# Optimization experiments

Hardware: AMD Instinct MI355X
Metric: run time of the kernel (lower is better)

The kernel has to match this reference:

```python
import jax, jax.numpy as jnp
import numpy as np

B = 512          # graphs
NODES = 90       # nodes per graph (fixed by lin1 = Linear(90*L*H, ...))
N = B * NODES    # total nodes
F_IN = 90        # dataset.num_features
H = 128          # hidden
L = 3            # num_layers
HL = 64          # hidden_linear
C = 2            # dataset.num_classes
DEG = 16         # avg degree
E = N * DEG      # total edges


def setup_inputs() -> dict:
    key = jax.random.key(0)
    ks = jax.random.split(key, 14)
    x = jax.random.normal(ks[0], (N, F_IN), jnp.float32)
    # intra-graph random edges: graph g owns nodes [g*90, (g+1)*90)
    g = jnp.repeat(jnp.arange(B), NODES * DEG)
    src = g * NODES + jax.random.randint(ks[1], (E,), 0, NODES)
    dst = g * NODES + jax.random.randint(ks[2], (E,), 0, NODES)
    edge_index = jnp.stack([src, dst]).astype(jnp.int64)
    edge_attr = jax.random.uniform(ks[3], (E,), jnp.float32, 0.1, 1.0)
    batch = jnp.repeat(jnp.arange(B), NODES).astype(jnp.int64)

    def lin(k, fi, fo):
        s = 1.0 / np.sqrt(fi)
        kw, kb = jax.random.split(k)
        return (jax.random.uniform(kw, (fi, fo), jnp.float32, -s, s),
                jax.random.uniform(kb, (fo,), jnp.float32, -s, s))

    W1, b1 = lin(ks[4], F_IN, H)
    W2, b2 = lin(ks[5], H, H)
    W3, b3 = lin(ks[6], H, H)
    lin1_W, lin1_b = lin(ks[7], NODES * L * H, HL)
    lin2_W, lin2_b = lin(ks[8], HL, C)
    return {"x": x, "edge_attr": edge_attr, "W1": W1, "b1": b1, "W2": W2,
            "b2": b2, "W3": W3, "b3": b3, "lin1_W": lin1_W, "lin1_b": lin1_b,
            "lin2_W": lin2_W, "lin2_b": lin2_b, "edge_index": edge_index,
            "batch": batch}


def reference(x, edge_attr, W1, b1, W2, b2, W3, b3, lin1_W, lin1_b,
              lin2_W, lin2_b, edge_index, batch):
    src, dst = edge_index[0], edge_index[1]
    # GCN normalization with added self-loops (weight 1), as in PyG GCNConv
    loop = jnp.arange(N)
    s = jnp.concatenate([src, loop])
    d = jnp.concatenate([dst, loop])
    w = jnp.concatenate([edge_attr, jnp.ones((N,), x.dtype)])
    deg = jax.ops.segment_sum(w, d, num_segments=N)
    dis = jnp.where(deg > 0, jax.lax.rsqrt(jnp.maximum(deg, 1e-30)), 0.0)
    norm = dis[s] * w * dis[d]  # [E+N]

    def conv(h, W, b):
        h = h @ W                                  # [N, H]
        msg = norm[:, None] * h[s]                 # gather+scale [E+N, H]
        return jax.ops.segment_sum(msg, d, num_segments=N) + b

    h1 = jax.nn.relu(conv(x, W1, b1))
    h2 = jax.nn.relu(conv(h1, W2, b2))
    h3 = jax.nn.relu(conv(h2, W3, b3))
    xc = jnp.concatenate([h1, h2, h3], axis=1)     # [N, L*H]
    # to_dense_batch: every graph has exactly 90 nodes in order, so no padding
    # (fill_value never appears) and dense batching is a pure reshape.
    z = xc.reshape(B, NODES * L * H)
    h = jax.nn.relu(z @ lin1_W + lin1_b)
    logits = h @ lin2_W + lin2_b                   # dropout is identity in eval
    return jax.nn.log_softmax(logits, axis=-1)
```

## Files before the change

kernel.cpp:

```cpp
#include <hip/hip_runtime.h>

typedef __bf16 bfx8 __attribute__((ext_vector_type(8)));
typedef float fx4 __attribute__((ext_vector_type(4)));
typedef unsigned short us4 __attribute__((ext_vector_type(4)));
typedef unsigned short us8 __attribute__((ext_vector_type(8)));

#define NNODES 90
#define NPAD   96
#define HF     128
#define NGRAPH 512
#define EPG    1440
#define ETOT   (NGRAPH*EPG)
#define KTOT   34560
#define NKTOT  1080
#define KSPLIT 45
#define KSTEPS (NKTOT/KSPLIT)

__device__ __forceinline__ float bf2f(unsigned short s){
  union { unsigned u; float f; } v; v.u = ((unsigned)s)<<16; return v.f;
}
__device__ __forceinline__ unsigned short f2bf(float f){
  union { float f; unsigned u; } v; v.f = f;
  return (unsigned short)((v.u + 0x7FFFu + ((v.u>>16)&1u)) >> 16);
}

__global__ void probe_kern(const unsigned short* __restrict__ x,
                           const int* __restrict__ ei,
                           int* __restrict__ flags){
  int t = threadIdx.x;
  __shared__ int sw[4];
  __shared__ long long se;
  int weird = 0;
  for (int i = t; i < 1024; i += 256) {
    unsigned u = x[i];
    int ex = (u >> 7) & 0xFF;
    if (ex > 157 || (ex < 97 && u != 0)) weird++;
  }
  for (int off = 32; off; off >>= 1) weird += __shfl_down(weird, off);
  if ((t & 63) == 0) sw[t >> 6] = weird;
  long long ss = 0;
  if (t < 64) { int v = ei[2*t + 1]; ss = (v < 0) ? -(long long)v : (long long)v; }
  for (int off = 32; off; off >>= 1) ss += __shfl_down(ss, off);
  if (t == 0) se = ss;
  __syncthreads();
  if (t == 0) {
    flags[0] = ((sw[0]+sw[1]+sw[2]+sw[3]) > 100) ? 1 : 0;
    flags[1] = (se == 0) ? 1 : 0;
  }
}

__global__ void pack_w3_kern(const unsigned short* __restrict__ W1,
                             const unsigned short* __restrict__ W2,
                             const unsigned short* __restrict__ W3,
                             unsigned short* __restrict__ o1,
                             unsigned short* __restrict__ o2,
                             unsigned short* __restrict__ o3,
                             const int* __restrict__ flags){
  int b = blockIdx.x;
  const unsigned short* W; unsigned short* out; int K, nK, t;
  if (b < 6)       { W = W1; out = o1; K = 90;  nK = 3; t = b*256 + threadIdx.x; }
  else if (b < 14) { W = W2; out = o2; K = 128; nK = 4; t = (b-6)*256 + threadIdx.x; }
  else             { W = W3; out = o3; K = 128; nK = 4; t = (b-14)*256 + threadIdx.x; }
  const int f32f = flags[0];
  const float* Wf = (const float*)W;
  int lane = t & 63;
  int ks = (t>>6) % nK;
  int nt = (t>>6) / nK;
  int n  = nt*16 + (lane&15);
  int k0 = ks*32 + (lane>>4)*8;
  unsigned short v[8];
#pragma unroll
  for (int j=0;j<8;j++){
    int k=k0+j;
    unsigned short val = 0;
    if (k < K) val = f32f ? f2bf(Wf[k*128+n]) : W[k*128+n];
    v[j] = val;
  }
  unsigned short* o = out + ((nt*nK+ks)*64 + lane)*8;
#pragma unroll
  for (int j=0;j<8;j++) o[j]=v[j];
}

__global__ void pack_lin1_kern(const unsigned short* __restrict__ W,
                               unsigned short* __restrict__ out,
                               const int* __restrict__ flags){
  __shared__ __align__(16) unsigned short tile[32*64];
  int ks = blockIdx.x;
  int t  = threadIdx.x;
  const int f32f = flags[0];
  if (f32f) {
    const float* Wf = (const float*)W;
#pragma unroll
    for (int j=0;j<8;j++) tile[t*8+j] = f2bf(Wf[ks*32*64 + t*8 + j]);
  } else {
    us8 v = *(const us8*)&W[ks*32*64 + t*8];
    *(us8*)&tile[t*8] = v;
  }
  __syncthreads();
  int lane = t & 63;
  int nt = t >> 6;
  int n  = nt*16 + (lane&15);
  int kq = (lane>>4)*8;
  us8 v;
#pragma unroll
  for (int j=0;j<8;j++) v[j] = tile[(kq+j)*64 + n];
  *(us8*)&out[((nt*NKTOT + ks)*64 + lane)*8] = v;
}

__global__ __launch_bounds__(512) void gcn_layers_kern(
    const unsigned short* __restrict__ x,
    const unsigned short* __restrict__ eattr,
    const int* __restrict__ ei,
    const unsigned short* __restrict__ w1p,
    const unsigned short* __restrict__ w2p,
    const unsigned short* __restrict__ w3p,
    const unsigned short* __restrict__ b1,
    const unsigned short* __restrict__ b2,
    const unsigned short* __restrict__ b3,
    unsigned short* __restrict__ xc,
    const int* __restrict__ flags)
{
  __shared__ __align__(16) char smem[65280];
  unsigned short* Abf = (unsigned short*)smem;
  unsigned short* H   = (unsigned short*)(smem + 17280);
  unsigned short* Tt  = (unsigned short*)(smem + 40320);
  float* Af  = (float*)(smem + 17280);
  float* deg = (float*)(smem + 64896);

  const int g = blockIdx.x;
  const int tid = threadIdx.x;
  const int lane = tid & 63, wave = tid >> 6;
  const int q = lane >> 4, r = lane & 15;
  const int eb = g*EPG;
  const int nb = g*NNODES;
  const int f32f = flags[0];
  const int i64f = flags[1];
  const float* xf = (const float*)x;
  const float* eaf = (const float*)eattr;
  const long long* e64 = (const long long*)ei;

  for (int i = tid; i < NNODES; i += 512) deg[i] = 1.0f;
  for (int i = tid; i < NNODES*NPAD; i += 512) Af[i] = 0.0f;
  __syncthreads();
  for (int e = tid; e < EPG; e += 512) {
    int d = (i64f ? (int)e64[ETOT + eb + e] : ei[ETOT + eb + e]) - nb;
    float w = f32f ? eaf[eb + e] : bf2f(eattr[eb + e]);
    atomicAdd(&deg[d], w);
  }
  __syncthreads();
  for (int i = tid; i < NNODES; i += 512) deg[i] = rsqrtf(deg[i]);
  __syncthreads();
  for (int e = tid; e < EPG; e += 512) {
    int s = (i64f ? (int)e64[eb + e] : ei[eb + e]) - nb;
    int d = (i64f ? (int)e64[ETOT + eb + e] : ei[ETOT + eb + e]) - nb;
    float w = f32f ? eaf[eb + e] : bf2f(eattr[eb + e]);
    atomicAdd(&Af[d*NPAD + s], deg[d]*w*deg[s]);
  }
  for (int i = tid; i < NNODES; i += 512) atomicAdd(&Af[i*NPAD + i], deg[i]*deg[i]);
  __syncthreads();
  for (int i = tid; i < NNODES*NPAD; i += 512) Abf[i] = f2bf(Af[i]);
  __syncthreads();
  for (int i = tid; i < NNODES*90; i += 512) {
    int node = i/90, f = i - node*90;
    H[node*HF + f] = f32f ? f2bf(xf[(nb + node)*90 + f]) : x[(nb + node)*90 + f];
  }
  for (int i = tid; i < NNODES*6; i += 512) {
    int node = i/6, c = i - node*6;
    H[node*HF + 90 + c] = 0;
  }
  __syncthreads();

#pragma unroll
  for (int l = 0; l < 3; ++l) {
    const unsigned short* wpk  = (l==0)? w1p : (l==1)? w2p : w3p;
    const unsigned short* bias = (l==0)? b1 : (l==1)? b2 : b3;
    const int nK = (l==0)? 3 : 4;

    {
      const int nt = wave;
      for (int mt = 0; mt < 6; ++mt) {
        int row = mt*16 + r; if (row > 89) row = 89;
        fx4 acc = {0.f,0.f,0.f,0.f};
#pragma unroll
        for (int ks = 0; ks < 4; ++ks)
          if (ks < nK) {
            bfx8 af = *(const bfx8*)(const void*)&H[row*HF + ks*32 + q*8];
            bfx8 bf = *(const bfx8*)(const void*)&wpk[((nt*nK + ks)*64 + lane)*8];
            acc = __builtin_amdgcn_mfma_f32_16x16x32_bf16(af, bf, acc, 0,0,0);
          }
        us4 o;
#pragma unroll
        for (int i2=0;i2<4;i2++) o[i2] = f2bf(acc[i2]);
        *(us4*)&Tt[(nt*16 + r)*NPAD + mt*16 + q*4] = o;
      }
    }
    __syncthreads();

    {
      const int ft = wave;
      bfx8 af[3];
#pragma unroll
      for (int ks = 0; ks < 3; ++ks)
        af[ks] = *(const bfx8*)(const void*)&Tt[(ft*16 + r)*NPAD + ks*32 + q*8];
      float bv[4];
#pragma unroll
      for (int i2=0;i2<4;i2++){
        int bidx = ft*16 + q*4 + i2;
        bv[i2] = f32f ? ((const float*)bias)[bidx] : bf2f(bias[bidx]);
      }
      for (int nt = 0; nt < 6; ++nt) {
        int arow = nt*16 + r; if (arow > 89) arow = 89;
        fx4 acc = {0.f,0.f,0.f,0.f};
#pragma unroll
        for (int ks = 0; ks < 3; ++ks) {
          bfx8 bfr = *(const bfx8*)(const void*)&Abf[arow*NPAD + ks*32 + q*8];
          acc = __builtin_amdgcn_mfma_f32_16x16x32_bf16(af[ks], bfr, acc, 0,0,0);
        }
        int m = nt*16 + r;
        if (m < NNODES) {
          us4 o;
#pragma unroll
          for (int i2=0;i2<4;i2++){
            float v = acc[i2] + bv[i2];
            o[i2] = f2bf(v > 0.f ? v : 0.f);
          }
          *(us4*)&H[m*HF + ft*16 + q*4] = o;
        }
      }
    }
    __syncthreads();

    for (int i = tid*4; i < NNODES*HF; i += 512*4) {
      us4 v = *(const us4*)&H[i];
      int node = i >> 7, f = i & 127;
      *(us4*)&xc[(nb + node)*384 + l*128 + f] = v;
    }
    __syncthreads();
  }
}

__global__ __launch_bounds__(256) void gemm2_kern(
    const unsigned short* __restrict__ z,
    const unsigned short* __restrict__ wp,
    float* __restrict__ accf)
{
  __shared__ __align__(16) unsigned short zt[32*128];
  int mb = blockIdx.x % 16;
  int kb = blockIdx.x / 16;
  int tid = threadIdx.x;
  int lane = tid & 63, wave = tid >> 6;
  int q = lane >> 4, r = lane & 15;
  int mt = wave >> 1;
  int nt0 = (wave & 1)*2;
  int m0 = mb*32;

  fx4 acc0 = {0,0,0,0}, acc1 = {0,0,0,0};
  int Lm = tid >> 3, Lc = tid & 7;
  int cA = Lc ^ (Lm & 7);
  int arow = mt*16 + r;

  for (int it = 0; it < KSTEPS/4; ++it) {
    int ks0 = kb*KSTEPS + it*4;
    int kbase = ks0*32;
    {
      us8 vA = *(const us8*)&z[(m0+Lm)*KTOT + kbase + cA*8];
      us8 vB = *(const us8*)&z[(m0+Lm)*KTOT + kbase + (cA+8)*8];
      *(us8*)&zt[Lm*128 + Lc*8] = vA;
      *(us8*)&zt[Lm*128 + (Lc+8)*8] = vB;
    }
    __syncthreads();
#pragma unroll
    for (int ks2 = 0; ks2 < 4; ++ks2) {
      int c = ks2*4 + q;
      int pos = (c & 8) | ((c & 7) ^ (arow & 7));
      bfx8 af = *(const bfx8*)(const void*)&zt[arow*128 + pos*8];
      int ksg = ks0 + ks2;
      bfx8 bA = *(const bfx8*)(const void*)&wp[(((nt0+0)*NKTOT + ksg)*64 + lane)*8];
      bfx8 bB = *(const bfx8*)(const void*)&wp[(((nt0+1)*NKTOT + ksg)*64 + lane)*8];
      acc0 = __builtin_amdgcn_mfma_f32_16x16x32_bf16(af, bA, acc0, 0,0,0);
      acc1 = __builtin_amdgcn_mfma_f32_16x16x32_bf16(af, bB, acc1, 0,0,0);
    }
    __syncthreads();
  }
#pragma unroll
  for (int i2 = 0; i2 < 4; ++i2) {
    int row = m0 + mt*16 + q*4 + i2;
    atomicAdd(&accf[row*64 + (nt0+0)*16 + r], acc0[i2]);
    atomicAdd(&accf[row*64 + (nt0+1)*16 + r], acc1[i2]);
  }
}

__global__ void head_kern(const float* __restrict__ accf,
                          const unsigned short* __restrict__ l1b,
                          const unsigned short* __restrict__ l2w,
                          const unsigned short* __restrict__ l2b,
                          unsigned short* __restrict__ out,
                          const int* __restrict__ flags)
{
  int gph = blockIdx.x;
  int j = threadIdx.x;
  const int f32f = flags[0];
  const float* l1bf = (const float*)l1b;
  const float* l2wf = (const float*)l2w;
  const float* l2bf = (const float*)l2b;
  float h = accf[gph*64 + j] + (f32f ? l1bf[j] : bf2f(l1b[j]));
  h = h > 0.f ? h : 0.f;
  float p0 = h * (f32f ? l2wf[2*j]   : bf2f(l2w[2*j]));
  float p1 = h * (f32f ? l2wf[2*j+1] : bf2f(l2w[2*j+1]));
  for (int off = 32; off; off >>= 1) {
    p0 += __shfl_down(p0, off);
    p1 += __shfl_down(p1, off);
  }
  if (j == 0) {
    float l0 = p0 + (f32f ? l2bf[0] : bf2f(l2b[0]));
    float l1 = p1 + (f32f ? l2bf[1] : bf2f(l2b[1]));
    float mx = fmaxf(l0, l1);
    float lse = mx + logf(expf(l0-mx) + expf(l1-mx));
    if (f32f) {
      ((float*)out)[gph*2]   = l0 - lse;
      ((float*)out)[gph*2+1] = l1 - lse;
    } else {
      out[gph*2]   = f2bf(l0 - lse);
      out[gph*2+1] = f2bf(l1 - lse);
    }
  }
}

extern "C" void kernel_launch(void* const* d_in, const int* in_sizes, int n_in,
                              void* d_out, int out_size, void* d_ws, size_t ws_size,
                              hipStream_t stream)
{
  const unsigned short* x   = (const unsigned short*)d_in[0];
  const unsigned short* ea  = (const unsigned short*)d_in[1];
  const unsigned short* W1  = (const unsigned short*)d_in[2];
  const unsigned short* b1  = (const unsigned short*)d_in[3];
  const unsigned short* W2  = (const unsigned short*)d_in[4];
  const unsigned short* b2  = (const unsigned short*)d_in[5];
  const unsigned short* W3  = (const unsigned short*)d_in[6];
  const unsigned short* b3  = (const unsigned short*)d_in[7];
  const unsigned short* L1W = (const unsigned short*)d_in[8];
  const unsigned short* L1b = (const unsigned short*)d_in[9];
  const unsigned short* L2W = (const unsigned short*)d_in[10];
  const unsigned short* L2b = (const unsigned short*)d_in[11];
  const int* ei             = (const int*)d_in[12];
  unsigned short* out       = (unsigned short*)d_out;

  char* ws = (char*)d_ws;
  unsigned short* xc  = (unsigned short*)(ws);
  unsigned short* l1p = (unsigned short*)(ws + 35389440);
  unsigned short* w1p = (unsigned short*)(ws + 39813120);
  unsigned short* w2p = (unsigned short*)(ws + 39837696);
  unsigned short* w3p = (unsigned short*)(ws + 39870464);
  float* accf         = (float*)(ws + 39903232);
  int* flags          = (int*)(ws + 40034304);

  probe_kern<<<1, 256, 0, stream>>>(x, ei, flags);
  pack_w3_kern<<<22, 256, 0, stream>>>(W1, W2, W3, w1p, w2p, w3p, flags);
  pack_lin1_kern<<<NKTOT, 256, 0, stream>>>(L1W, l1p, flags);
  gcn_layers_kern<<<NGRAPH, 512, 0, stream>>>(x, ea, ei, w1p, w2p, w3p,
                                              b1, b2, b3, xc, flags);
  hipMemsetAsync(accf, 0, NGRAPH*64*sizeof(float), stream);
  gemm2_kern<<<16*KSPLIT, 256, 0, stream>>>(xc, l1p, accf);
  head_kern<<<NGRAPH, 64, 0, stream>>>(accf, L1b, L2W, L2b, out, flags);
}
```

Measured before the change: 171.5 us.

## Merge pack kernels, drop dtype probe, swizzle H, prefetch gemm2 tiles

Removes the runtime dtype probe kernel and fixes inputs as fp32. The weight-pack kernels and the accumulator memset are merged into one launch. In the GCN kernel, the edge lists are loaded once into registers and the degree and adjacency atomics are fused, with normalization applied when converting to bf16. H uses an XOR-swizzled LDS layout to avoid bank conflicts, and per-layer weights are hoisted into registers. The lin1 GEMM register-prefetches the next z tile, and the head kernel packs 4 graphs per block. Fewer launches and less LDS contention are the aim. The cost is dropping the bf16 input path.

```diff
diff --git a/kernel.cpp b/kernel.cpp
--- a/kernel.cpp
+++ b/kernel.cpp
@@ -16,109 +16,79 @@
 #define KSPLIT 45
 #define KSTEPS (NKTOT/KSPLIT)
 
-__device__ __forceinline__ float bf2f(unsigned short s){
-  union { unsigned u; float f; } v; v.u = ((unsigned)s)<<16; return v.f;
-}
 __device__ __forceinline__ unsigned short f2bf(float f){
   union { float f; unsigned u; } v; v.f = f;
   return (unsigned short)((v.u + 0x7FFFu + ((v.u>>16)&1u)) >> 16);
 }
-
-__global__ void probe_kern(const unsigned short* __restrict__ x,
-                           const int* __restrict__ ei,
-                           int* __restrict__ flags){
+__device__ __forceinline__ int hsw(int node, int f){
+  return node*HF + ((((f>>3) ^ (node&15)))<<3) + (f&7);
+}
+
+__global__ __launch_bounds__(256) void pack_all_kern(
+    const float* __restrict__ W1,
+    const float* __restrict__ W2,
+    const float* __restrict__ W3,
+    const float* __restrict__ L1W,
+    unsigned short* __restrict__ o1,
+    unsigned short* __restrict__ o2,
+    unsigned short* __restrict__ o3,
+    unsigned short* __restrict__ l1p,
+    float* __restrict__ accf)
+{
+  __shared__ __align__(16) unsigned short tile[32*64];
+  int b = blockIdx.x;
   int t = threadIdx.x;
-  __shared__ int sw[4];
-  __shared__ long long se;
-  int weird = 0;
-  for (int i = t; i < 1024; i += 256) {
-    unsigned u = x[i];
-    int ex = (u >> 7) & 0xFF;
-    if (ex > 157 || (ex < 97 && u != 0)) weird++;
-  }
-  for (int off = 32; off; off >>= 1) weird += __shfl_down(weird, off);
-  if ((t & 63) == 0) sw[t >> 6] = weird;
-  long long ss = 0;
-  if (t < 64) { int v = ei[2*t + 1]; ss = (v < 0) ? -(long long)v : (long long)v; }
-  for (int off = 32; off; off >>= 1) ss += __shfl_down(ss, off);
-  if (t == 0) se = ss;
-  __syncthreads();
-  if (t == 0) {
-    flags[0] = ((sw[0]+sw[1]+sw[2]+sw[3]) > 100) ? 1 : 0;
-    flags[1] = (se == 0) ? 1 : 0;
-  }
-}
-
-__global__ void pack_w3_kern(const unsigned short* __restrict__ W1,
-                             const unsigned short* __restrict__ W2,
-                             const unsigned short* __restrict__ W3,
-                             unsigned short* __restrict__ o1,
-                             unsigned short* __restrict__ o2,
-                             unsigned short* __restrict__ o3,
-                             const int* __restrict__ flags){
-  int b = blockIdx.x;
-  const unsigned short* W; unsigned short* out; int K, nK, t;
-  if (b < 6)       { W = W1; out = o1; K = 90;  nK = 3; t = b*256 + threadIdx.x; }
-  else if (b < 14) { W = W2; out = o2; K = 128; nK = 4; t = (b-6)*256 + threadIdx.x; }
-  else             { W = W3; out = o3; K = 128; nK = 4; t = (b-14)*256 + threadIdx.x; }
-  const int f32f = flags[0];
-  const float* Wf = (const float*)W;
-  int lane = t & 63;
-  int ks = (t>>6) % nK;
-  int nt = (t>>6) / nK;
-  int n  = nt*16 + (lane&15);
-  int k0 = ks*32 + (lane>>4)*8;
-  unsigned short v[8];
-#pragma unroll
-  for (int j=0;j<8;j++){
-    int k=k0+j;
-    unsigned short val = 0;
-    if (k < K) val = f32f ? f2bf(Wf[k*128+n]) : W[k*128+n];
-    v[j] = val;
-  }
-  unsigned short* o = out + ((nt*nK+ks)*64 + lane)*8;
-#pragma unroll
-  for (int j=0;j<8;j++) o[j]=v[j];
-}
-
-__global__ void pack_lin1_kern(const unsigned short* __restrict__ W,
-                               unsigned short* __restrict__ out,
-                               const int* __restrict__ flags){
-  __shared__ __align__(16) unsigned short tile[32*64];
-  int ks = blockIdx.x;
-  int t  = threadIdx.x;
-  const int f32f = flags[0];
-  if (f32f) {
-    const float* Wf = (const float*)W;
-#pragma unroll
-    for (int j=0;j<8;j++) tile[t*8+j] = f2bf(Wf[ks*32*64 + t*8 + j]);
+  if (b < NKTOT) {
+    int ks = b;
+#pragma unroll
+    for (int j=0;j<8;j++) tile[t*8+j] = f2bf(L1W[ks*32*64 + t*8 + j]);
+    __syncthreads();
+    int lane = t & 63;
+    int nt = t >> 6;
+    int n  = nt*16 + (lane&15);
+    int kq = (lane>>4)*8;
+    us8 v;
+#pragma unroll
+    for (int j=0;j<8;j++) v[j] = tile[(kq+j)*64 + n];
+    *(us8*)&l1p[((nt*NKTOT + ks)*64 + lane)*8] = v;
+  } else if (b < NKTOT + 22) {
+    int bb = b - NKTOT;
+    const float* W; unsigned short* out; int K, nK, tt;
+    if (bb < 6)       { W = W1; out = o1; K = 90;  nK = 3; tt = bb*256 + t; }
+    else if (bb < 14) { W = W2; out = o2; K = 128; nK = 4; tt = (bb-6)*256 + t; }
+    else              { W = W3; out = o3; K = 128; nK = 4; tt = (bb-14)*256 + t; }
+    int lane = tt & 63;
+    int ks = (tt>>6) % nK;
+    int nt = (tt>>6) / nK;
+    int n  = nt*16 + (lane&15);
+    int k0 = ks*32 + (lane>>4)*8;
+    unsigned short v[8];
+#pragma unroll
+    for (int j=0;j<8;j++){ int k=k0+j; v[j] = (k<K)? f2bf(W[k*128+n]) : (unsigned short)0; }
+    unsigned short* o = out + ((nt*nK+ks)*64 + lane)*8;
+#pragma unroll
+    for (int j=0;j<8;j++) o[j]=v[j];
   } else {
-    us8 v = *(const us8*)&W[ks*32*64 + t*8];
-    *(us8*)&tile[t*8] = v;
-  }
-  __syncthreads();
-  int lane = t & 63;
-  int nt = t >> 6;
-  int n  = nt*16 + (lane&15);
-  int kq = (lane>>4)*8;
-  us8 v;
-#pragma unroll
-  for (int j=0;j<8;j++) v[j] = tile[(kq+j)*64 + n];
-  *(us8*)&out[((nt*NKTOT + ks)*64 + lane)*8] = v;
+    int base = (b - (NKTOT+22))*16384 + t*4;
+#pragma unroll
+    for (int i = 0; i < 16; ++i) {
+      fx4 z = {0.f,0.f,0.f,0.f};
+      *(fx4*)&accf[base + i*1024] = z;
+    }
+  }
 }
 
 __global__ __launch_bounds__(512) void gcn_layers_kern(
-    const unsigned short* __restrict__ x,
-    const unsigned short* __restrict__ eattr,
+    const float* __restrict__ x,
+    const float* __restrict__ eattr,
     const int* __restrict__ ei,
     const unsigned short* __restrict__ w1p,
     const unsigned short* __restrict__ w2p,
     const unsigned short* __restrict__ w3p,
-    const unsigned short* __restrict__ b1,
-    const unsigned short* __restrict__ b2,
-    const unsigned short* __restrict__ b3,
-    unsigned short* __restrict__ xc,
-    const int* __restrict__ flags)
+    const float* __restrict__ b1,
+    const float* __restrict__ b2,
+    const float* __restrict__ b3,
+    unsigned short* __restrict__ xc)
 {
   __shared__ __align__(16) char smem[65280];
   unsigned short* Abf = (unsigned short*)smem;
@@ -133,88 +103,98 @@
   const int q = lane >> 4, r = lane & 15;
   const int eb = g*EPG;
   const int nb = g*NNODES;
-  const int f32f = flags[0];
-  const int i64f = flags[1];
-  const float* xf = (const float*)x;
-  const float* eaf = (const float*)eattr;
   const long long* e64 = (const long long*)ei;
 
-  for (int i = tid; i < NNODES; i += 512) deg[i] = 1.0f;
+  bool i64f;
+  {
+    int v = ei[2*lane + 1];
+    i64f = (__ballot(v != 0) == 0ull);
+  }
+
+  const int e0 = tid, e1 = tid + 512, e2 = tid + 1024;
+  const bool h2 = (e2 < EPG);
+  int s0, d0, s1, d1, s2 = nb, d2 = nb;
+  if (i64f) {
+    s0 = (int)e64[eb+e0]; d0 = (int)e64[ETOT+eb+e0];
+    s1 = (int)e64[eb+e1]; d1 = (int)e64[ETOT+eb+e1];
+    if (h2) { s2 = (int)e64[eb+e2]; d2 = (int)e64[ETOT+eb+e2]; }
+  } else {
+    s0 = ei[eb+e0]; d0 = ei[ETOT+eb+e0];
+    s1 = ei[eb+e1]; d1 = ei[ETOT+eb+e1];
+    if (h2) { s2 = ei[eb+e2]; d2 = ei[ETOT+eb+e2]; }
+  }
+  float w0 = eattr[eb+e0];
+  float w1 = eattr[eb+e1];
+  float w2 = h2 ? eattr[eb+e2] : 0.f;
+
+  for (int i = tid; i < NPAD; i += 512) deg[i] = 1.0f;
   for (int i = tid; i < NNODES*NPAD; i += 512) Af[i] = 0.0f;
   __syncthreads();
-  for (int e = tid; e < EPG; e += 512) {
-    int d = (i64f ? (int)e64[ETOT + eb + e] : ei[ETOT + eb + e]) - nb;
-    float w = f32f ? eaf[eb + e] : bf2f(eattr[eb + e]);
-    atomicAdd(&deg[d], w);
-  }
-  __syncthreads();
-  for (int i = tid; i < NNODES; i += 512) deg[i] = rsqrtf(deg[i]);
-  __syncthreads();
-  for (int e = tid; e < EPG; e += 512) {
-    int s = (i64f ? (int)e64[eb + e] : ei[eb + e]) - nb;
-    int d = (i64f ? (int)e64[ETOT + eb + e] : ei[ETOT + eb + e]) - nb;
-    float w = f32f ? eaf[eb + e] : bf2f(eattr[eb + e]);
-    atomicAdd(&Af[d*NPAD + s], deg[d]*w*deg[s]);
-  }
-  for (int i = tid; i < NNODES; i += 512) atomicAdd(&Af[i*NPAD + i], deg[i]*deg[i]);
-  __syncthreads();
-  for (int i = tid; i < NNODES*NPAD; i += 512) Abf[i] = f2bf(Af[i]);
+  atomicAdd(&Af[(d0-nb)*NPAD + (s0-nb)], w0); atomicAdd(&deg[d0-nb], w0);
+  atomicAdd(&Af[(d1-nb)*NPAD + (s1-nb)], w1); atomicAdd(&deg[d1-nb], w1);
+  if (h2) { atomicAdd(&Af[(d2-nb)*NPAD + (s2-nb)], w2); atomicAdd(&deg[d2-nb], w2); }
+  __syncthreads();
+  for (int i = tid; i < NPAD; i += 512) deg[i] = rsqrtf(deg[i]);
+  __syncthreads();
+  for (int i = tid; i < NNODES*NPAD; i += 512) {
+    int row = i / NPAD, col = i - row*NPAD;
+    float a = Af[i];
+    if (col == row) a += 1.0f;
+    Abf[i] = f2bf(a * deg[row] * deg[col]);
+  }
   __syncthreads();
   for (int i = tid; i < NNODES*90; i += 512) {
     int node = i/90, f = i - node*90;
-    H[node*HF + f] = f32f ? f2bf(xf[(nb + node)*90 + f]) : x[(nb + node)*90 + f];
+    H[hsw(node, f)] = f2bf(x[(nb + node)*90 + f]);
   }
   for (int i = tid; i < NNODES*6; i += 512) {
-    int node = i/6, c = i - node*6;
-    H[node*HF + 90 + c] = 0;
+    int node = i/6, f = 90 + (i - node*6);
+    H[hsw(node, f)] = 0;
   }
   __syncthreads();
 
 #pragma unroll
   for (int l = 0; l < 3; ++l) {
-    const unsigned short* wpk  = (l==0)? w1p : (l==1)? w2p : w3p;
-    const unsigned short* bias = (l==0)? b1 : (l==1)? b2 : b3;
+    const unsigned short* wpk = (l==0)? w1p : (l==1)? w2p : w3p;
+    const float* bias         = (l==0)? b1 : (l==1)? b2 : b3;
     const int nK = (l==0)? 3 : 4;
 
+    bfx8 wf[4];
+#pragma unroll
+    for (int ks = 0; ks < 4; ++ks)
+      if (ks < nK) wf[ks] = *(const bfx8*)(const void*)&wpk[((wave*nK + ks)*64 + lane)*8];
+
+    for (int mt = 0; mt < 6; ++mt) {
+      int row = mt*16 + r; if (row > 89) row = 89;
+      fx4 acc = {0.f,0.f,0.f,0.f};
+#pragma unroll
+      for (int ks = 0; ks < 4; ++ks)
+        if (ks < nK) {
+          bfx8 af = *(const bfx8*)(const void*)&H[row*HF + (((4*ks + q) ^ (row&15))<<3)];
+          acc = __builtin_amdgcn_mfma_f32_16x16x32_bf16(af, wf[ks], acc, 0,0,0);
+        }
+      us4 o;
+#pragma unroll
+      for (int i2=0;i2<4;i2++) o[i2] = f2bf(acc[i2]);
+      *(us4*)&Tt[(wave*16 + r)*NPAD + mt*16 + q*4] = o;
+    }
+    __syncthreads();
+
     {
-      const int nt = wave;
-      for (int mt = 0; mt < 6; ++mt) {
-        int row = mt*16 + r; if (row > 89) row = 89;
-        fx4 acc = {0.f,0.f,0.f,0.f};
-#pragma unroll
-        for (int ks = 0; ks < 4; ++ks)
-          if (ks < nK) {
-            bfx8 af = *(const bfx8*)(const void*)&H[row*HF + ks*32 + q*8];
-            bfx8 bf = *(const bfx8*)(const void*)&wpk[((nt*nK + ks)*64 + lane)*8];
-            acc = __builtin_amdgcn_mfma_f32_16x16x32_bf16(af, bf, acc, 0,0,0);
-          }
-        us4 o;
-#pragma unroll
-        for (int i2=0;i2<4;i2++) o[i2] = f2bf(acc[i2]);
-        *(us4*)&Tt[(nt*16 + r)*NPAD + mt*16 + q*4] = o;
-      }
-    }
-    __syncthreads();
-
-    {
-      const int ft = wave;
-      bfx8 af[3];
+      bfx8 tf[3];
 #pragma unroll
       for (int ks = 0; ks < 3; ++ks)
-        af[ks] = *(const bfx8*)(const void*)&Tt[(ft*16 + r)*NPAD + ks*32 + q*8];
+        tf[ks] = *(const bfx8*)(const void*)&Tt[(wave*16 + r)*NPAD + ks*32 + q*8];
       float bv[4];
 #pragma unroll
-      for (int i2=0;i2<4;i2++){
-        int bidx = ft*16 + q*4 + i2;
-        bv[i2] = f32f ? ((const float*)bias)[bidx] : bf2f(bias[bidx]);
-      }
+      for (int i2=0;i2<4;i2++) bv[i2] = bias[wave*16 + q*4 + i2];
       for (int nt = 0; nt < 6; ++nt) {
         int arow = nt*16 + r; if (arow > 89) arow = 89;
         fx4 acc = {0.f,0.f,0.f,0.f};
 #pragma unroll
         for (int ks = 0; ks < 3; ++ks) {
           bfx8 bfr = *(const bfx8*)(const void*)&Abf[arow*NPAD + ks*32 + q*8];
-          acc = __builtin_amdgcn_mfma_f32_16x16x32_bf16(af[ks], bfr, acc, 0,0,0);
+          acc = __builtin_amdgcn_mfma_f32_16x16x32_bf16(tf[ks], bfr, acc, 0,0,0);
         }
         int m = nt*16 + r;
         if (m < NNODES) {
@@ -224,18 +204,17 @@
             float v = acc[i2] + bv[i2];
             o[i2] = f2bf(v > 0.f ? v : 0.f);
           }
-          *(us4*)&H[m*HF + ft*16 + q*4] = o;
+          *(us4*)&H[m*HF + (((2*wave + (q>>1)) ^ (m&15))<<3) + (q&1)*4] = o;
         }
       }
     }
     __syncthreads();
 
     for (int i = tid*4; i < NNODES*HF; i += 512*4) {
-      us4 v = *(const us4*)&H[i];
       int node = i >> 7, f = i & 127;
+      us4 v = *(const us4*)&H[node*HF + (((f>>3) ^ (node&15))<<3) + (f&7)];
       *(us4*)&xc[(nb + node)*384 + l*128 + f] = v;
     }
-    __syncthreads();
   }
 }
 
@@ -258,17 +237,21 @@
   int Lm = tid >> 3, Lc = tid & 7;
   int cA = Lc ^ (Lm & 7);
   int arow = mt*16 + r;
+  const unsigned short* zrow = &z[(m0+Lm)*KTOT];
+
+  us8 pvA = *(const us8*)&zrow[kb*KSTEPS*32 + cA*8];
+  us8 pvB = *(const us8*)&zrow[kb*KSTEPS*32 + (cA+8)*8];
 
   for (int it = 0; it < KSTEPS/4; ++it) {
+    *(us8*)&zt[Lm*128 + Lc*8] = pvA;
+    *(us8*)&zt[Lm*128 + (Lc+8)*8] = pvB;
+    __syncthreads();
+    if (it < KSTEPS/4 - 1) {
+      int kn = (kb*KSTEPS + (it+1)*4)*32;
+      pvA = *(const us8*)&zrow[kn + cA*8];
+      pvB = *(const us8*)&zrow[kn + (cA+8)*8];
+    }
     int ks0 = kb*KSTEPS + it*4;
-    int kbase = ks0*32;
-    {
-      us8 vA = *(const us8*)&z[(m0+Lm)*KTOT + kbase + cA*8];
-      us8 vB = *(const us8*)&z[(m0+Lm)*KTOT + kbase + (cA+8)*8];
-      *(us8*)&zt[Lm*128 + Lc*8] = vA;
-      *(us8*)&zt[Lm*128 + (Lc+8)*8] = vB;
-    }
-    __syncthreads();
 #pragma unroll
     for (int ks2 = 0; ks2 < 4; ++ks2) {
       int c = ks2*4 + q;
@@ -290,39 +273,30 @@
   }
 }
 
-__global__ void head_kern(const float* __restrict__ accf,
-                          const unsigned short* __restrict__ l1b,
-                          const unsigned short* __restrict__ l2w,
-                          const unsigned short* __restrict__ l2b,
-                          unsigned short* __restrict__ out,
-                          const int* __restrict__ flags)
-{
-  int gph = blockIdx.x;
-  int j = threadIdx.x;
-  const int f32f = flags[0];
-  const float* l1bf = (const float*)l1b;
-  const float* l2wf = (const float*)l2w;
-  const float* l2bf = (const float*)l2b;
-  float h = accf[gph*64 + j] + (f32f ? l1bf[j] : bf2f(l1b[j]));
+__global__ __launch_bounds__(256) void head_kern(
+    const float* __restrict__ accf,
+    const float* __restrict__ l1b,
+    const float* __restrict__ l2w,
+    const float* __restrict__ l2b,
+    float* __restrict__ out)
+{
+  int gph = blockIdx.x*4 + (threadIdx.x >> 6);
+  int j = threadIdx.x & 63;
+  float h = accf[gph*64 + j] + l1b[j];
   h = h > 0.f ? h : 0.f;
-  float p0 = h * (f32f ? l2wf[2*j]   : bf2f(l2w[2*j]));
-  float p1 = h * (f32f ? l2wf[2*j+1] : bf2f(l2w[2*j+1]));
+  float p0 = h * l2w[2*j];
+  float p1 = h * l2w[2*j+1];
   for (int off = 32; off; off >>= 1) {
     p0 += __shfl_down(p0, off);
     p1 += __shfl_down(p1, off);
   }
   if (j == 0) {
-    float l0 = p0 + (f32f ? l2bf[0] : bf2f(l2b[0]));
-    float l1 = p1 + (f32f ? l2bf[1] : bf2f(l2b[1]));
+    float l0 = p0 + l2b[0];
+    float l1 = p1 + l2b[1];
     float mx = fmaxf(l0, l1);
     float lse = mx + logf(expf(l0-mx) + expf(l1-mx));
-    if (f32f) {
-      ((float*)out)[gph*2]   = l0 - lse;
-      ((float*)out)[gph*2+1] = l1 - lse;
-    } else {
-      out[gph*2]   = f2bf(l0 - lse);
-      out[gph*2+1] = f2bf(l1 - lse);
-    }
+    out[gph*2]   = l0 - lse;
+    out[gph*2+1] = l1 - lse;
   }
 }
 
@@ -330,20 +304,20 @@
                               void* d_out, int out_size, void* d_ws, size_t ws_size,
                               hipStream_t stream)
 {
-  const unsigned short* x   = (const unsigned short*)d_in[0];
-  const unsigned short* ea  = (const unsigned short*)d_in[1];
-  const unsigned short* W1  = (const unsigned short*)d_in[2];
-  const unsigned short* b1  = (const unsigned short*)d_in[3];
-  const unsigned short* W2  = (const unsigned short*)d_in[4];
-  const unsigned short* b2  = (const unsigned short*)d_in[5];
-  const unsigned short* W3  = (const unsigned short*)d_in[6];
-  const unsigned short* b3  = (const unsigned short*)d_in[7];
-  const unsigned short* L1W = (const unsigned short*)d_in[8];
-  const unsigned short* L1b = (const unsigned short*)d_in[9];
-  const unsigned short* L2W = (const unsigned short*)d_in[10];
-  const unsigned short* L2b = (const unsigned short*)d_in[11];
-  const int* ei             = (const int*)d_in[12];
-  unsigned short* out       = (unsigned short*)d_out;
+  const float* x   = (const float*)d_in[0];
+  const float* ea  = (const float*)d_in[1];
+  const float* W1  = (const float*)d_in[2];
+  const float* b1  = (const float*)d_in[3];
+  const float* W2  = (const float*)d_in[4];
+  const float* b2  = (const float*)d_in[5];
+  const float* W3  = (const float*)d_in[6];
+  const float* b3  = (const float*)d_in[7];
+  const float* L1W = (const float*)d_in[8];
+  const float* L1b = (const float*)d_in[9];
+  const float* L2W = (const float*)d_in[10];
+  const float* L2b = (const float*)d_in[11];
+  const int* ei    = (const int*)d_in[12];
+  float* out       = (float*)d_out;
 
   char* ws = (char*)d_ws;
   unsigned short* xc  = (unsigned short*)(ws);
@@ -352,14 +326,11 @@
   unsigned short* w2p = (unsigned short*)(ws + 39837696);
   unsigned short* w3p = (unsigned short*)(ws + 39870464);
   float* accf         = (float*)(ws + 39903232);
-  int* flags          = (int*)(ws + 40034304);
-
-  probe_kern<<<1, 256, 0, stream>>>(x, ei, flags);
-  pack_w3_kern<<<22, 256, 0, stream>>>(W1, W2, W3, w1p, w2p, w3p, flags);
-  pack_lin1_kern<<<NKTOT, 256, 0, stream>>>(L1W, l1p, flags);
+
+  pack_all_kern<<<NKTOT + 22 + 2, 256, 0, stream>>>(W1, W2, W3, L1W,
+                                                    w1p, w2p, w3p, l1p, accf);
   gcn_layers_kern<<<NGRAPH, 512, 0, stream>>>(x, ea, ei, w1p, w2p, w3p,
-                                              b1, b2, b3, xc, flags);
-  hipMemsetAsync(accf, 0, NGRAPH*64*sizeof(float), stream);
+                                              b1, b2, b3, xc);
   gemm2_kern<<<16*KSPLIT, 256, 0, stream>>>(xc, l1p, accf);
-  head_kern<<<NGRAPH, 64, 0, stream>>>(accf, L1b, L2W, L2b, out, flags);
-}
+  head_kern<<<NGRAPH/4, 256, 0, stream>>>(accf, L1b, L2W, L2b, out);
+}
```

After: 143.9 us. -16.1%, faster.
